# Optimization experiments

Measured on AMD Instinct MI355X. Metric: run time of the kernel, lower is better.

The kernel has to match this reference:

```python
import jax, jax.numpy as jnp
import numpy as np

B, S, DIM, H, HD = 4, 1024, 1280, 16, 80
SCALE = HD ** -0.5
ROPE_THETA = 10000.0


def rotate_half(x):
    x1, x2 = jnp.split(x, 2, axis=-1)
    return jnp.concatenate([-x2, x1], axis=-1)


def setup_inputs() -> dict:
    key = jax.random.key(0)
    ks = jax.random.split(key, 5)
    x = jax.random.normal(ks[0], (B, S, DIM), dtype=jnp.float32)
    Wqkv = jax.random.normal(ks[1], (DIM, 3 * DIM), dtype=jnp.float32) * 0.02
    bqkv = jax.random.normal(ks[2], (3 * DIM,), dtype=jnp.float32) * 0.01
    Wproj = jax.random.normal(ks[3], (DIM, DIM), dtype=jnp.float32) * 0.02
    bproj = jax.random.normal(ks[4], (DIM,), dtype=jnp.float32) * 0.01
    # realistic rotary tables: (S, HD) with duplicated freq halves (matches rotate_half layout)
    inv_freq = 1.0 / (ROPE_THETA ** (jnp.arange(0, HD, 2, dtype=jnp.float32) / HD))
    freqs = jnp.outer(jnp.arange(S, dtype=jnp.float32), inv_freq)  # (S, HD/2)
    emb = jnp.concatenate([freqs, freqs], axis=-1)  # (S, HD)
    rope_cos = jnp.cos(emb)
    rope_sin = jnp.sin(emb)
    return {"x": x, "rope_cos": rope_cos, "rope_sin": rope_sin,
            "Wqkv": Wqkv, "bqkv": bqkv, "Wproj": Wproj, "bproj": bproj}


def reference(x, rope_cos, rope_sin, Wqkv, bqkv, Wproj, bproj):
    b, s, d = x.shape
    qkv = (x @ Wqkv + bqkv).reshape(b, s, 3, H, HD)
    q, k, v = qkv[:, :, 0], qkv[:, :, 1], qkv[:, :, 2]  # each (b, s, H, HD)
    cos = rope_cos[None, :, None, :]  # (1, s, 1, HD)
    sin = rope_sin[None, :, None, :]
    q = q * cos + rotate_half(q) * sin
    k = k * cos + rotate_half(k) * sin
    # SDPA with all-ones mask (full attention)
    scores = jnp.einsum("bqhd,bkhd->bhqk", q, k) * SCALE
    probs = jax.nn.softmax(scores, axis=-1)
    out = jnp.einsum("bhqk,bkhd->bqhd", probs, v).reshape(b, s, d)
    return out @ Wproj + bproj
```

## Files before the change

kernel.cpp:

```cpp
#include <hip/hip_runtime.h>
#include <math.h>

#define SCALE_F 0.11180339887498949f
#define HDP 96

typedef short  short8  __attribute__((ext_vector_type(8)));
typedef short  short4v __attribute__((ext_vector_type(4)));
typedef float  f32x4   __attribute__((ext_vector_type(4)));
typedef __bf16 bf16x8  __attribute__((ext_vector_type(8)));

__device__ __forceinline__ float bf2f(short s) {
  union { unsigned u; float f; } v;
  v.u = ((unsigned)(unsigned short)s) << 16;
  return v.f;
}
__device__ __forceinline__ short f2b(float f) {
  __bf16 h = (__bf16)f;
  return __builtin_bit_cast(short, h);
}
__device__ __forceinline__ bool probe_is_bf16(const unsigned* probe) {
  return (probe[1] & 0xFFFFu) != 0u;
}
__device__ __forceinline__ float load_scalar(const void* p, int i, bool isb) {
  return isb ? bf2f(((const short*)p)[i]) : ((const float*)p)[i];
}

__device__ __forceinline__ void gload_lds16(const short* g, short* l) {
  __builtin_amdgcn_global_load_lds(
      (const __attribute__((address_space(1))) void*)g,
      (__attribute__((address_space(3))) void*)l, 16, 0, 0);
}

template <typename V>
__device__ __forceinline__ auto mfma_try(V a, V b, f32x4 c, int)
    -> decltype(__builtin_amdgcn_mfma_f32_16x16x32_bf16(a, b, c, 0, 0, 0)) {
  return __builtin_amdgcn_mfma_f32_16x16x32_bf16(a, b, c, 0, 0, 0);
}
template <typename V>
__device__ __forceinline__ f32x4 mfma_try(V a, V b, f32x4 c, long) {
  return __builtin_amdgcn_mfma_f32_16x16x32_bf16(
      __builtin_bit_cast(bf16x8, a), __builtin_bit_cast(bf16x8, b), c, 0, 0, 0);
}
__device__ __forceinline__ f32x4 MFMA(short8 a, short8 b, f32x4 c) {
  return mfma_try(a, b, c, 0);
}

__global__ __launch_bounds__(256) void cvt_x_kernel(
    const void* __restrict__ xin, short* __restrict__ xout,
    const unsigned* __restrict__ probe) {
  bool isb = probe_is_bf16(probe);
  size_t i = ((size_t)blockIdx.x * 256 + threadIdx.x) * 8;
  if (isb) {
    *(short8*)&xout[i] = *(const short8*)((const short*)xin + i);
  } else {
    const float* f = (const float*)xin + i;
    float4 a0 = *(const float4*)f;
    float4 a1 = *(const float4*)(f + 4);
    short8 sv;
    sv[0] = f2b(a0.x); sv[1] = f2b(a0.y); sv[2] = f2b(a0.z); sv[3] = f2b(a0.w);
    sv[4] = f2b(a1.x); sv[5] = f2b(a1.y); sv[6] = f2b(a1.z); sv[7] = f2b(a1.w);
    *(short8*)&xout[i] = sv;
  }
}

__global__ __launch_bounds__(256) void transpose_kernel(
    const void* __restrict__ in, short* __restrict__ out, int R, int C,
    const unsigned* __restrict__ probe) {
  bool isb = probe_is_bf16(probe);
  __shared__ float tile[32][33];
  int t = threadIdx.x;
  int bx = blockIdx.x;
  int by = blockIdx.y;
  int r = t >> 3, c4 = (t & 7) * 4;
  size_t idx = (size_t)(by * 32 + r) * C + bx * 32 + c4;
  if (isb) {
    short4v v = *(const short4v*)((const short*)in + idx);
    tile[r][c4 + 0] = bf2f(v[0]);
    tile[r][c4 + 1] = bf2f(v[1]);
    tile[r][c4 + 2] = bf2f(v[2]);
    tile[r][c4 + 3] = bf2f(v[3]);
  } else {
    float4 v = *(const float4*)((const float*)in + idx);
    tile[r][c4 + 0] = v.x;
    tile[r][c4 + 1] = v.y;
    tile[r][c4 + 2] = v.z;
    tile[r][c4 + 3] = v.w;
  }
  __syncthreads();
  int rr = t >> 3, k4 = (t & 7) * 4;
  short4v o;
  o[0] = f2b(tile[k4 + 0][rr]);
  o[1] = f2b(tile[k4 + 1][rr]);
  o[2] = f2b(tile[k4 + 2][rr]);
  o[3] = f2b(tile[k4 + 3][rr]);
  *(short4v*)&out[(size_t)(bx * 32 + rr) * R + by * 32 + k4] = o;
}

__global__ __launch_bounds__(512, 2) void gemm_qkv_kernel(
    const short* __restrict__ X, const short* __restrict__ Wt,
    const void* __restrict__ bias, const unsigned* __restrict__ probe,
    short* __restrict__ Qw, short* __restrict__ Kw, short* __restrict__ Vt) {
  const int K = 1280;
  __shared__ short Al[2][2][8192];
  __shared__ short Bl[2][2][8192];
  int t = threadIdx.x;
  int bm = blockIdx.x / 15, bn = blockIdx.x % 15;
  int m0 = bm * 256, n0 = bn * 256;
  int w = t >> 6, lane = t & 63;
  int quad = lane >> 4, l16 = lane & 15, l8 = l16 & 7;
  int arow = (w >> 2) * 64 + l16;
  int brow = (w & 3) * 32 + l16;
  int sr = t >> 3, t8s = t * 8;
  int sjs = (t & 7) ^ (sr & 7);
  int soff0 = ((quad ^ l8) * 8);
  int soff1 = (((4 + quad) ^ l8) * 8);
  f32x4 acc[2][2][4][2] = {};

#define STAGE8(PTR, R0, KOFF, LP)                                            \
  {                                                                          \
    const short* g_ = (PTR) + (size_t)((R0) + sr) * 1280 + (KOFF) + sjs * 8; \
    gload_lds16(g_, (LP) + t8s);                                             \
    gload_lds16(g_ + 64 * 1280, (LP) + t8s + 4096);                          \
  }

#define PHASE(S, HA, HB, QM, QN, STAGE_CODE, DO_VW)                          \
  {                                                                          \
    short8 af[4][2], bfv[2][2];                                              \
    _Pragma("unroll") for (int mt = 0; mt < 4; mt++) {                       \
      int rp_ = (arow + mt * 16) * 64;                                       \
      af[mt][0] = *(const short8*)&Al[S][HA][rp_ + soff0];                   \
      af[mt][1] = *(const short8*)&Al[S][HA][rp_ + soff1];                   \
    }                                                                        \
    _Pragma("unroll") for (int nt = 0; nt < 2; nt++) {                       \
      int rp_ = (brow + nt * 16) * 64;                                       \
      bfv[nt][0] = *(const short8*)&Bl[S][HB][rp_ + soff0];                  \
      bfv[nt][1] = *(const short8*)&Bl[S][HB][rp_ + soff1];                  \
    }                                                                        \
    STAGE_CODE;                                                              \
    __builtin_amdgcn_s_barrier();                                            \
    asm volatile("s_waitcnt lgkmcnt(0)" ::: "memory");                       \
    __builtin_amdgcn_sched_barrier(0);                                       \
    __builtin_amdgcn_s_setprio(1);                                           \
    _Pragma("unroll") for (int mt = 0; mt < 4; mt++)                         \
      _Pragma("unroll") for (int nt = 0; nt < 2; nt++) {                     \
        acc[QM][QN][mt][nt] = MFMA(af[mt][0], bfv[nt][0], acc[QM][QN][mt][nt]); \
        acc[QM][QN][mt][nt] = MFMA(af[mt][1], bfv[nt][1], acc[QM][QN][mt][nt]); \
      }                                                                      \
    __builtin_amdgcn_s_setprio(0);                                           \
    if (DO_VW) {                                                             \
      asm volatile("s_waitcnt vmcnt(4)" ::: "memory");                       \
      __builtin_amdgcn_sched_barrier(0);                                     \
    }                                                                        \
    __builtin_amdgcn_s_barrier();                                            \
  }

  STAGE8(X,  m0,       0,  &Al[0][0][0]);
  STAGE8(X,  m0 + 128, 0,  &Al[0][1][0]);
  STAGE8(Wt, n0,       0,  &Bl[0][0][0]);
  STAGE8(Wt, n0 + 128, 0,  &Bl[0][1][0]);
  STAGE8(X,  m0,       64, &Al[1][0][0]);
  STAGE8(Wt, n0,       64, &Bl[1][0][0]);
  asm volatile("s_waitcnt vmcnt(4)" ::: "memory");
  __builtin_amdgcn_sched_barrier(0);
  __builtin_amdgcn_s_barrier();

  for (int i = 0; i < 10; i++) {
    int k1 = (2 * i + 1) * 64;
    int k2 = (2 * i + 2) * 64; if (k2 >= K) k2 = 0;
    int k3 = (2 * i + 3) * 64; if (k3 >= K) k3 = 0;
    PHASE(0, 0, 0, 0, 0, STAGE8(X,  m0 + 128, k1, &Al[1][1][0]), 0);
    PHASE(0, 0, 1, 0, 1, STAGE8(Wt, n0 + 128, k1, &Bl[1][1][0]), 0);
    PHASE(0, 1, 0, 1, 0, STAGE8(X,  m0,       k2, &Al[0][0][0]), 0);
    PHASE(0, 1, 1, 1, 1, STAGE8(Wt, n0,       k2, &Bl[0][0][0]), 1);
    PHASE(1, 0, 0, 0, 0, STAGE8(X,  m0 + 128, k2, &Al[0][1][0]), 0);
    PHASE(1, 0, 1, 0, 1, STAGE8(Wt, n0 + 128, k2, &Bl[0][1][0]), 0);
    PHASE(1, 1, 0, 1, 0, STAGE8(X,  m0,       k3, &Al[1][0][0]), 0);
    PHASE(1, 1, 1, 1, 1, STAGE8(Wt, n0,       k3, &Bl[1][0][0]), 1);
  }
  asm volatile("s_waitcnt vmcnt(0)" ::: "memory");
  __builtin_amdgcn_sched_barrier(0);

  bool isb = probe_is_bf16(probe);
  float bv[2][2];
#pragma unroll
  for (int qn = 0; qn < 2; qn++)
#pragma unroll
    for (int nt = 0; nt < 2; nt++)
      bv[qn][nt] =
          load_scalar(bias, n0 + qn * 128 + (w & 3) * 32 + nt * 16 + l16, isb);
#pragma unroll
  for (int qm = 0; qm < 2; qm++)
#pragma unroll
    for (int mt = 0; mt < 4; mt++) {
      int mbase = m0 + qm * 128 + (w >> 2) * 64 + mt * 16 + quad * 4;
      int b = mbase >> 10, sbase = mbase & 1023;
#pragma unroll
      for (int qn = 0; qn < 2; qn++)
#pragma unroll
        for (int nt = 0; nt < 2; nt++) {
          int n = n0 + qn * 128 + (w & 3) * 32 + nt * 16 + l16;
          int which = n / 1280;
          int rmod = n - which * 1280;
          int h = rmod / 80;
          int d = rmod - h * 80;
          int bh = b * 16 + h;
          if (which == 2) {
            short4v vv;
#pragma unroll
            for (int reg = 0; reg < 4; reg++)
              vv[reg] = f2b(acc[qm][qn][mt][nt][reg] + bv[qn][nt]);
            *(short4v*)&Vt[((size_t)bh * 80 + d) * 1024 + sbase] = vv;
          } else {
            short* dst = (which == 0 ? Qw : Kw);
#pragma unroll
            for (int reg = 0; reg < 4; reg++)
              dst[((size_t)bh * 1024 + sbase + reg) * HDP + d] =
                  f2b(acc[qm][qn][mt][nt][reg] + bv[qn][nt]);
          }
        }
    }
#undef PHASE
#undef STAGE8
}

__global__ __launch_bounds__(256) void rope_kernel(
    short* __restrict__ Qw, short* __restrict__ Kw,
    const void* __restrict__ cosb, const void* __restrict__ sinb,
    const unsigned* __restrict__ probe) {
  bool isb = probe_is_bf16(probe);
  int t = threadIdx.x;
  int w = t >> 6, lane = t & 63;
  int job = blockIdx.x * 4 + w;
  int which = job & 1;
  int row = job >> 1;
  int s = row & 1023;
  short* ptr = (which ? Kw : Qw) + (size_t)row * HDP;
  float scale = which ? 1.0f : SCALE_F;
  if (lane < 40) {
    float p0 = bf2f(ptr[lane]);
    float p1 = bf2f(ptr[lane + 40]);
    float c0 = load_scalar(cosb, s * 80 + lane, isb);
    float s0 = load_scalar(sinb, s * 80 + lane, isb);
    float c1 = load_scalar(cosb, s * 80 + lane + 40, isb);
    float s1 = load_scalar(sinb, s * 80 + lane + 40, isb);
    ptr[lane] = f2b((p0 * c0 - p1 * s0) * scale);
    ptr[lane + 40] = f2b((p1 * c1 + p0 * s1) * scale);
  } else if (lane < 56) {
    ptr[40 + lane] = 0;
  }
}

__global__ __launch_bounds__(256) void attn_kernel(
    const short* __restrict__ Qw, const short* __restrict__ Kw,
    const short* __restrict__ Vt, short* __restrict__ out) {
  __shared__ short Klds[64 * 104];
  __shared__ short Vlds[80 * 72];
  __shared__ short Ps[4][16 * 72];
  int t = threadIdx.x;
  int w = t >> 6, lane = t & 63;
  int quad = lane >> 4, l16 = lane & 15;
  int bh = blockIdx.x & 63;
  int qt = blockIdx.x >> 6;
  int q0 = qt * 64;
  const short* Kb = Kw + (size_t)bh * 1024 * HDP;
  const short* Vb = Vt + (size_t)bh * 80 * 1024;

  short8 aq[3];
  {
    const short* qrow = Qw + ((size_t)bh * 1024 + q0 + w * 16 + l16) * HDP;
#pragma unroll
    for (int ks = 0; ks < 3; ks++)
      aq[ks] = *(const short8*)&qrow[ks * 32 + quad * 8];
  }

  short8 kreg[3], vreg[3];
#define PREFETCH(c)                                                        \
  {                                                                        \
    _Pragma("unroll") for (int i = 0; i < 3; i++) {                        \
      int idx = i * 256 + t;                                               \
      int row = idx / 12, col = (idx % 12) * 8;                            \
      kreg[i] = *(const short8*)&Kb[(size_t)((c) + row) * HDP + col];      \
    }                                                                      \
    _Pragma("unroll") for (int i = 0; i < 3; i++) {                        \
      int idx = i * 256 + t;                                               \
      if (idx < 640) {                                                     \
        int d = idx >> 3, s0 = (idx & 7) * 8;                              \
        vreg[i] = *(const short8*)&Vb[(size_t)d * 1024 + (c) + s0];        \
      }                                                                    \
    }                                                                      \
  }
#define STORE_LDS()                                                        \
  {                                                                        \
    _Pragma("unroll") for (int i = 0; i < 3; i++) {                        \
      int idx = i * 256 + t;                                               \
      int row = idx / 12, col = (idx % 12) * 8;                            \
      *(short8*)&Klds[row * 104 + col] = kreg[i];                          \
    }                                                                      \
    _Pragma("unroll") for (int i = 0; i < 3; i++) {                        \
      int idx = i * 256 + t;                                               \
      if (idx < 640) {                                                     \
        int d = idx >> 3, s0 = (idx & 7) * 8;                              \
        *(short8*)&Vlds[d * 72 + s0] = vreg[i];                            \
      }                                                                    \
    }                                                                      \
  }

  PREFETCH(0);
  STORE_LDS();
  __syncthreads();

  f32x4 ofr[5] = {};
  float lsum[4] = {0.f, 0.f, 0.f, 0.f};
  short* Pw = &Ps[w][0];

  for (int c = 0; c < 1024; c += 64) {
    if (c + 64 < 1024) PREFETCH(c + 64);
    f32x4 sf[4] = {};
#pragma unroll
    for (int nt = 0; nt < 4; nt++) {
      short8 bk0 = *(const short8*)&Klds[(nt * 16 + l16) * 104 + 0 * 32 + quad * 8];
      short8 bk1 = *(const short8*)&Klds[(nt * 16 + l16) * 104 + 1 * 32 + quad * 8];
      short8 bk2 = *(const short8*)&Klds[(nt * 16 + l16) * 104 + 2 * 32 + quad * 8];
      sf[nt] = MFMA(aq[0], bk0, sf[nt]);
      sf[nt] = MFMA(aq[1], bk1, sf[nt]);
      sf[nt] = MFMA(aq[2], bk2, sf[nt]);
    }
#pragma unroll
    for (int r = 0; r < 4; r++) {
      float p0 = __expf(fminf(sf[0][r], 30.f));
      float p1 = __expf(fminf(sf[1][r], 30.f));
      float p2 = __expf(fminf(sf[2][r], 30.f));
      float p3 = __expf(fminf(sf[3][r], 30.f));
      sf[0][r] = p0; sf[1][r] = p1; sf[2][r] = p2; sf[3][r] = p3;
      lsum[r] += (p0 + p1) + (p2 + p3);
    }
#pragma unroll
    for (int nt = 0; nt < 4; nt++)
#pragma unroll
      for (int r = 0; r < 4; r++)
        Pw[(quad * 4 + r) * 72 + nt * 16 + l16] = f2b(sf[nt][r]);
    __threadfence_block();
    short8 ap[2];
#pragma unroll
    for (int ks = 0; ks < 2; ks++)
      ap[ks] = *(const short8*)&Pw[l16 * 72 + ks * 32 + quad * 8];
#pragma unroll
    for (int nt = 0; nt < 5; nt++) {
      short8 bv0 = *(const short8*)&Vlds[(nt * 16 + l16) * 72 + 0 * 32 + quad * 8];
      short8 bv1 = *(const short8*)&Vlds[(nt * 16 + l16) * 72 + 1 * 32 + quad * 8];
      ofr[nt] = MFMA(ap[0], bv0, ofr[nt]);
      ofr[nt] = MFMA(ap[1], bv1, ofr[nt]);
    }
    __syncthreads();
    if (c + 64 < 1024) {
      STORE_LDS();
      __syncthreads();
    }
  }
#pragma unroll
  for (int off = 1; off < 16; off <<= 1)
#pragma unroll
    for (int r = 0; r < 4; r++) lsum[r] += __shfl_xor(lsum[r], off);
  float inv[4];
#pragma unroll
  for (int r = 0; r < 4; r++) inv[r] = 1.f / lsum[r];
  int b = bh >> 4, h = bh & 15;
#pragma unroll
  for (int nt = 0; nt < 5; nt++) {
    int d = nt * 16 + l16;
#pragma unroll
    for (int r = 0; r < 4; r++) {
      int s = q0 + w * 16 + quad * 4 + r;
      out[((size_t)(b * 1024 + s)) * 1280 + h * 80 + d] = f2b(ofr[nt][r] * inv[r]);
    }
  }
}

__global__ __launch_bounds__(256) void gemm_proj_kernel(
    const short* __restrict__ A, const short* __restrict__ Wt,
    const void* __restrict__ bias, const unsigned* __restrict__ probe,
    float* __restrict__ out) {
  const int K = 1280;
  __shared__ short As[2][128 * 32];
  __shared__ short Bs[2][128 * 32];
  int t = threadIdx.x;
  int bm = blockIdx.x / 10;
  int bn = blockIdx.x % 10;
  int m0 = bm * 128, n0 = bn * 128;
  int w = t >> 6, lane = t & 63;
  int wm = w & 1, wn = w >> 1;
  int quad = lane >> 4, l16 = lane & 15;
  int row = t >> 2, ch = (t & 3) * 8, row2 = row + 64;
  int t8 = t * 8;
  const short* Ar  = A  + (size_t)(m0 + row)  * K + ch;
  const short* Ar2 = A  + (size_t)(m0 + row2) * K + ch;
  const short* Wr  = Wt + (size_t)(n0 + row)  * K + ch;
  const short* Wr2 = Wt + (size_t)(n0 + row2) * K + ch;
  f32x4 acc[4][4] = {};
  gload_lds16(Ar,  &As[0][t8]);
  gload_lds16(Ar2, &As[0][t8 + 2048]);
  gload_lds16(Wr,  &Bs[0][t8]);
  gload_lds16(Wr2, &Bs[0][t8 + 2048]);
  __syncthreads();
  int p = 0;
#define PROJ_COMPUTE(pp)                                                      \
  {                                                                           \
    short8 af[4], bfr[4];                                                     \
    _Pragma("unroll") for (int mt = 0; mt < 4; mt++)                          \
        af[mt] = *(const short8*)&As[pp][(wm * 64 + mt * 16 + l16) * 32 + quad * 8]; \
    _Pragma("unroll") for (int nt = 0; nt < 4; nt++)                          \
        bfr[nt] = *(const short8*)&Bs[pp][(wn * 64 + nt * 16 + l16) * 32 + quad * 8]; \
    _Pragma("unroll") for (int mt = 0; mt < 4; mt++)                          \
        _Pragma("unroll") for (int nt = 0; nt < 4; nt++)                      \
            acc[mt][nt] = MFMA(af[mt], bfr[nt], acc[mt][nt]);                 \
  }
  for (int k0 = 32; k0 < K; k0 += 32, p ^= 1) {
    gload_lds16(Ar + k0,  &As[p ^ 1][t8]);
    gload_lds16(Ar2 + k0, &As[p ^ 1][t8 + 2048]);
    gload_lds16(Wr + k0,  &Bs[p ^ 1][t8]);
    gload_lds16(Wr2 + k0, &Bs[p ^ 1][t8 + 2048]);
    PROJ_COMPUTE(p);
    __syncthreads();
  }
  PROJ_COMPUTE(p);
  bool isb = probe_is_bf16(probe);
  float bv[4];
#pragma unroll
  for (int nt = 0; nt < 4; nt++)
    bv[nt] = load_scalar(bias, n0 + wn * 64 + nt * 16 + l16, isb);
#pragma unroll
  for (int mt = 0; mt < 4; mt++) {
#pragma unroll
    for (int nt = 0; nt < 4; nt++) {
      int n = n0 + wn * 64 + nt * 16 + l16;
#pragma unroll
      for (int reg = 0; reg < 4; reg++) {
        int m = m0 + wm * 64 + mt * 16 + quad * 4 + reg;
        out[(size_t)m * 1280 + n] = acc[mt][nt][reg] + bv[nt];
      }
    }
  }
}

extern "C" void kernel_launch(void* const* d_in, const int* in_sizes, int n_in,
                              void* d_out, int out_size, void* d_ws, size_t ws_size,
                              hipStream_t stream) {
  const void* x        = d_in[0];
  const void* rope_cos = d_in[1];
  const void* rope_sin = d_in[2];
  const void* Wqkv     = d_in[3];
  const void* bqkv     = d_in[4];
  const void* Wproj    = d_in[5];
  const void* bproj    = d_in[6];
  const unsigned* probe = (const unsigned*)rope_cos;
  char* ws = (char*)d_ws;
  short* Wt1 = (short*)(ws + 0);
  short* Wt2 = (short*)(ws + 9830400);
  short* Qw  = (short*)(ws + 13107200);
  short* Kw  = (short*)(ws + 25690112);
  short* Vt  = (short*)(ws + 38273024);
  short* Xb  = (short*)(ws + 48758784);
  short* At  = (short*)(ws + 48758784);

  cvt_x_kernel<<<2560, 256, 0, stream>>>(x, Xb, probe);
  transpose_kernel<<<dim3(3840 / 32, 1280 / 32), 256, 0, stream>>>(Wqkv, Wt1, 1280, 3840, probe);
  transpose_kernel<<<dim3(1280 / 32, 1280 / 32), 256, 0, stream>>>(Wproj, Wt2, 1280, 1280, probe);
  gemm_qkv_kernel<<<240, 512, 0, stream>>>(Xb, Wt1, bqkv, probe, Qw, Kw, Vt);
  rope_kernel<<<32768, 256, 0, stream>>>(Qw, Kw, rope_cos, rope_sin, probe);
  attn_kernel<<<1024, 256, 0, stream>>>(Qw, Kw, Vt, At);
  gemm_proj_kernel<<<32 * 10, 256, 0, stream>>>(At, Wt2, bproj, probe, (float*)d_out);
}
```

Measured before the change: 262.0 us.

## Double attention query tile to 128 rows with 8 waves per block

The attention kernel now runs 512 threads (8 waves) per block, each block covering 128 query rows instead of 64, and launches half as many blocks. Each K/V tile staged in LDS is shared by twice as many waves, which halves global K/V traffic per query and the per-block load work. The prefetch and store code is rewritten for the 512-thread layout. In exchange, per-block LDS grows, the launch-bounds hint changes, there are fewer blocks to spread across CUs, and every barrier now waits on more waves.

After: 244.4 us. 1.07x faster.

```diff
diff --git a/kernel.cpp b/kernel.cpp
--- a/kernel.cpp
+++ b/kernel.cpp
@@ -250,18 +250,18 @@
   }
 }
 
-__global__ __launch_bounds__(256) void attn_kernel(
+__global__ __launch_bounds__(512, 4) void attn_kernel(
     const short* __restrict__ Qw, const short* __restrict__ Kw,
     const short* __restrict__ Vt, short* __restrict__ out) {
   __shared__ short Klds[64 * 104];
   __shared__ short Vlds[80 * 72];
-  __shared__ short Ps[4][16 * 72];
+  __shared__ short Ps[8][16 * 72];
   int t = threadIdx.x;
   int w = t >> 6, lane = t & 63;
   int quad = lane >> 4, l16 = lane & 15;
   int bh = blockIdx.x & 63;
   int qt = blockIdx.x >> 6;
-  int q0 = qt * 64;
+  int q0 = qt * 128;
   const short* Kb = Kw + (size_t)bh * 1024 * HDP;
   const short* Vb = Vt + (size_t)bh * 80 * 1024;
 
@@ -273,35 +273,47 @@
       aq[ks] = *(const short8*)&qrow[ks * 32 + quad * 8];
   }
 
-  short8 kreg[3], vreg[3];
+  short8 kreg[2], vreg[2];
 #define PREFETCH(c)                                                        \
   {                                                                        \
-    _Pragma("unroll") for (int i = 0; i < 3; i++) {                        \
-      int idx = i * 256 + t;                                               \
+    {                                                                      \
+      int row = t / 12, col = (t % 12) * 8;                                \
+      kreg[0] = *(const short8*)&Kb[(size_t)((c) + row) * HDP + col];      \
+    }                                                                      \
+    if (t < 256) {                                                         \
+      int idx = 512 + t;                                                   \
       int row = idx / 12, col = (idx % 12) * 8;                            \
-      kreg[i] = *(const short8*)&Kb[(size_t)((c) + row) * HDP + col];      \
-    }                                                                      \
-    _Pragma("unroll") for (int i = 0; i < 3; i++) {                        \
-      int idx = i * 256 + t;                                               \
-      if (idx < 640) {                                                     \
-        int d = idx >> 3, s0 = (idx & 7) * 8;                              \
-        vreg[i] = *(const short8*)&Vb[(size_t)d * 1024 + (c) + s0];        \
-      }                                                                    \
+      kreg[1] = *(const short8*)&Kb[(size_t)((c) + row) * HDP + col];      \
+    }                                                                      \
+    {                                                                      \
+      int d = t >> 3, s0 = (t & 7) * 8;                                    \
+      vreg[0] = *(const short8*)&Vb[(size_t)d * 1024 + (c) + s0];          \
+    }                                                                      \
+    if (t < 128) {                                                         \
+      int idx = 512 + t;                                                   \
+      int d = idx >> 3, s0 = (idx & 7) * 8;                                \
+      vreg[1] = *(const short8*)&Vb[(size_t)d * 1024 + (c) + s0];          \
     }                                                                      \
   }
 #define STORE_LDS()                                                        \
   {                                                                        \
-    _Pragma("unroll") for (int i = 0; i < 3; i++) {                        \
-      int idx = i * 256 + t;                                               \
+    {                                                                      \
+      int row = t / 12, col = (t % 12) * 8;                                \
+      *(short8*)&Klds[row * 104 + col] = kreg[0];                          \
+    }                                                                      \
+    if (t < 256) {                                                         \
+      int idx = 512 + t;                                                   \
       int row = idx / 12, col = (idx % 12) * 8;                            \
-      *(short8*)&Klds[row * 104 + col] = kreg[i];                          \
-    }                                                                      \
-    _Pragma("unroll") for (int i = 0; i < 3; i++) {                        \
-      int idx = i * 256 + t;                                               \
-      if (idx < 640) {                                                     \
-        int d = idx >> 3, s0 = (idx & 7) * 8;                              \
-        *(short8*)&Vlds[d * 72 + s0] = vreg[i];                            \
-      }                                                                    \
+      *(short8*)&Klds[row * 104 + col] = kreg[1];                          \
+    }                                                                      \
+    {                                                                      \
+      int d = t >> 3, s0 = (t & 7) * 8;                                    \
+      *(short8*)&Vlds[d * 72 + s0] = vreg[0];                              \
+    }                                                                      \
+    if (t < 128) {                                                         \
+      int idx = 512 + t;                                                   \
+      int d = idx >> 3, s0 = (idx & 7) * 8;                                \
+      *(short8*)&Vlds[d * 72 + s0] = vreg[1];                              \
     }                                                                      \
   }
 
@@ -467,6 +479,6 @@
   transpose_kernel<<<dim3(1280 / 32, 1280 / 32), 256, 0, stream>>>(Wproj, Wt2, 1280, 1280, probe);
   gemm_qkv_kernel<<<240, 512, 0, stream>>>(Xb, Wt1, bqkv, probe, Qw, Kw, Vt);
   rope_kernel<<<32768, 256, 0, stream>>>(Qw, Kw, rope_cos, rope_sin, probe);
-  attn_kernel<<<1024, 256, 0, stream>>>(Qw, Kw, Vt, At);
+  attn_kernel<<<512, 512, 0, stream>>>(Qw, Kw, Vt, At);
   gemm_proj_kernel<<<32 * 10, 256, 0, stream>>>(At, Wt2, bproj, probe, (float*)d_out);
 }
```
